# Kernel optimization log

Hardware: AMD Instinct MI355X
Metric: run time of the kernel (lower is better)

The kernel has to match this reference:

```python
import jax, jax.numpy as jnp
import numpy as np

H = 1024   # hidden_dim
L = 2      # n_layers
B = 50     # batch (hardcoded via positions expand)
S = 457    # coords length (hardcoded arange)
T = 32     # maxlen['txt']
V = 27     # dict_size


def gru_cell(x, h, Wih, Whh, bih, bhh):
    # PyTorch GRU cell math. x: (B, in), h: (B, H)
    gi = x @ Wih.T + bih
    gh = h @ Whh.T + bhh
    ir, iz, inn = jnp.split(gi, 3, axis=-1)
    hr, hz, hn = jnp.split(gh, 3, axis=-1)
    r = jax.nn.sigmoid(ir + hr)
    z = jax.nn.sigmoid(iz + hz)
    n = jnp.tanh(inn + r * hn)
    return (1.0 - z) * n + z * h


def setup_inputs() -> dict:
    key = jax.random.key(0)
    ks = iter(jax.random.split(key, 32))
    p = lambda shape: jax.random.normal(next(ks), shape, dtype=jnp.float32) * 0.05
    inp = {
        'x': jax.random.normal(next(ks), (B, 2, S), dtype=jnp.float32),
        'emb': p((V, H)),
        # encoder GRU (layer0 input=3, layer1 input=H)
        'enc_Wih0': p((3 * H, 3)), 'enc_Whh0': p((3 * H, H)),
        'enc_bih0': p((3 * H,)),   'enc_bhh0': p((3 * H,)),
        'enc_Wih1': p((3 * H, H)), 'enc_Whh1': p((3 * H, H)),
        'enc_bih1': p((3 * H,)),   'enc_bhh1': p((3 * H,)),
        # decoder GRU, stacked over layers (all inputs are H)
        'dec_Wih': p((L, 3 * H, H)), 'dec_Whh': p((L, 3 * H, H)),
        'dec_bih': p((L, 3 * H)),    'dec_bhh': p((L, 3 * H)),
        # attention_fc: Linear(2H, H) + ReLU ; fc: Linear(H, V)
        'attn_W': p((H, 2 * H)), 'attn_b': p((H,)),
        'fc_W': p((V, H)),       'fc_b': p((V,)),
    }
    return inp


def reference(x, emb, enc_Wih0, enc_Whh0, enc_bih0, enc_bhh0,
              enc_Wih1, enc_Whh1, enc_bih1, enc_bhh1,
              dec_Wih, dec_Whh, dec_bih, dec_bhh,
              attn_W, attn_b, fc_W, fc_b):
    # ----- encoder -----
    pos = jnp.broadcast_to(jnp.arange(S, dtype=x.dtype)[None, :, None], (B, S, 1))
    inp = jnp.concatenate([jnp.transpose(x, (0, 2, 1)), pos], axis=-1)  # (B,S,3)
    seq = jnp.transpose(inp, (1, 0, 2))  # (S,B,3) time-major for scan
    h0 = jnp.zeros((B, H), x.dtype)
    hiddens = []
    for (Wih, Whh, bih, bhh) in ((enc_Wih0, enc_Whh0, enc_bih0, enc_bhh0),
                                 (enc_Wih1, enc_Whh1, enc_bih1, enc_bhh1)):
        def step(h, xt, Wih=Wih, Whh=Whh, bih=bih, bhh=bhh):
            h2 = gru_cell(xt, h, Wih, Whh, bih, bhh)
            return h2, h2
        hT, seq = jax.lax.scan(step, h0, seq)
        hiddens.append(hT)
    enc_outs = jnp.transpose(seq, (1, 0, 2))  # (B,S,H)
    hidden = jnp.stack(hiddens)               # (L,B,H)

    def dec_step(carry, _):
        vec_in, hid = carry
        x_t = emb[vec_in]  # (B,H)
        new_h = []
        inp_t = x_t
        for l in range(L):
            hl = gru_cell(inp_t, hid[l], dec_Wih[l], dec_Whh[l], dec_bih[l], dec_bhh[l])
            new_h.append(hl)
            inp_t = hl
        out_t = inp_t  # (B,H)
        score = jnp.einsum('bsh,bh->bs', enc_outs, out_t)      # bmm(v, q)
        w = jax.nn.softmax(score, axis=1)                      # softmax over S
        a = jnp.einsum('bsh,bs->bh', enc_outs, w)              # bmm(v^T, w)
        comb = jnp.concatenate([out_t, a], axis=-1)            # (B,2H)
        hfc = jax.nn.relu(comb @ attn_W.T + attn_b)
        logits = hfc @ fc_W.T + fc_b                           # (B,V)
        nv = jnp.argmax(logits, axis=-1).astype(jnp.int32)
        return (nv, jnp.stack(new_h)), (logits, w)

    init = (jnp.zeros((B,), jnp.int32), hidden)
    (_, hid_f), (logits_seq, w_seq) = jax.lax.scan(dec_step, init, None, length=T)
    vec_out = jnp.transpose(logits_seq, (1, 0, 2))  # (B,T,V)
    attn_w = jnp.transpose(w_seq, (1, 2, 0))        # (B,S,T)
    return vec_out, hid_f, attn_w
```

## Files before the change

### kernel.cpp

```cpp
#include <hip/hip_runtime.h>
#include <math.h>

#define HD 1024
#define BB 50
#define SS 457
#define TT 32
#define VV 27

#define SSTR 68
#define WSTR 68

enum { G_ENC0 = 0, G_GRU = 1, G_SCR = 2, G_SCRGATE = 3, G_RELU = 4 };

struct Role {
  const float* srcA; const float* srcB;
  const float* Wa;   const float* Wb;
  const float* bih;  const float* bhh;
  const float* hv;   const float* scr;
  float* out; float* out2; float* scrw;
  int strA, strB, wstrA, K, gate, rowsLinear, gatherA, nsA, nsB;
};

__global__ __launch_bounds__(256) void fused_gemm(
    Role r0, Role r1, int split, int skipRole, int p,
    const float* __restrict__ x, const float* __restrict__ Wih0,
    const float* __restrict__ emb, const int* __restrict__ tok)
{
  __shared__ __align__(16) float Sk[64][SSTR];
  __shared__ __align__(16) float Wt[12][WSTR];
  __shared__ __align__(16) float part[4][16][4][4][4];

  const int blk = blockIdx.x;
  const int roleId = split ? (blk & 1) : 0;
  if (roleId == skipRole) return;
  const Role& R = roleId ? r1 : r0;
  const int bi2 = split ? (blk >> 1) : blk;
  const int j0 = bi2 * (R.rowsLinear ? 12 : 4);

  const int tid = threadIdx.x;
  const int tx = tid & 3;
  const int ty = (tid >> 2) & 15;
  const int kh = tid >> 6;

  float aR[4] = {0,0,0,0}, aZ[4] = {0,0,0,0}, aN2[4] = {0,0,0,0}, aN3[4] = {0,0,0,0};

  const int nit = R.K >> 6;

  for (int it = 0; it < nit; ++it) {
    const int kw = it << 6;
    const bool second = (R.srcB != nullptr) && (kw >= 1024);
    const int kloc = second ? (kw - 1024) : kw;

    float4 sv[4];
#pragma unroll
    for (int u = 0; u < 4; ++u) {
      int e = tid + (u << 8);
      int b = e >> 4, f4 = e & 15;
      int bc = b < BB ? b : BB - 1;
      const float* rp;
      if (second)         rp = R.srcB + (size_t)bc * R.strB + kloc;
      else if (R.gatherA) rp = emb + (size_t)tok[bc] * HD + kw;
      else                rp = R.srcA + (size_t)bc * R.strA + kw;
      sv[u] = *(const float4*)(rp + (f4 << 2));
    }
    float4 wv = make_float4(0.f, 0.f, 0.f, 0.f);
    if (tid < 192) {
      int r = tid >> 4, f4 = tid & 15;
      int wrow;
      if (R.rowsLinear) { int j = j0 + r; wrow = j < 1024 ? j : 1023; }
      else { int g = r >> 2, jj = r & 3; int j = j0 + jj; if (j > 1023) j = 1023;
             wrow = g * 1024 + j; }
      const float* wp = second ? (R.Wb + (size_t)wrow * 1024 + kloc)
                               : (R.Wa + (size_t)wrow * R.wstrA + kw);
      wv = *(const float4*)(wp + (f4 << 2));
    }

    __syncthreads();
#pragma unroll
    for (int u = 0; u < 4; ++u) {
      int e = tid + (u << 8);
      int b = e >> 4, f4 = e & 15;
      int k = f4 << 2;
      Sk[k + 0][b] = sv[u].x;
      Sk[k + 1][b] = sv[u].y;
      Sk[k + 2][b] = sv[u].z;
      Sk[k + 3][b] = sv[u].w;
    }
    if (tid < 192) {
      int r = tid >> 4, f4 = tid & 15;
      *(float4*)&Wt[r][f4 << 2] = wv;
    }
    __syncthreads();

    const bool ns2 = second ? (R.nsB == 2) : (R.nsA == 2);
#define FMA4(A, wc, s) { A[0] = fmaf(wc, s.x, A[0]); A[1] = fmaf(wc, s.y, A[1]); \
                         A[2] = fmaf(wc, s.z, A[2]); A[3] = fmaf(wc, s.w, A[3]); }
#define CBLOCK(AN) \
    _Pragma("unroll") \
    for (int k4 = 0; k4 < 4; ++k4) { \
      const int kk = (kh << 4) + (k4 << 2); \
      float4 w0 = *(const float4*)&Wt[tx][kk]; \
      float4 w1 = *(const float4*)&Wt[4 + tx][kk]; \
      float4 w2 = *(const float4*)&Wt[8 + tx][kk]; \
      float4 s0 = *(const float4*)&Sk[kk + 0][ty << 2]; \
      float4 s1 = *(const float4*)&Sk[kk + 1][ty << 2]; \
      float4 s2 = *(const float4*)&Sk[kk + 2][ty << 2]; \
      float4 s3 = *(const float4*)&Sk[kk + 3][ty << 2]; \
      FMA4(aR, w0.x, s0) FMA4(aR, w0.y, s1) FMA4(aR, w0.z, s2) FMA4(aR, w0.w, s3) \
      FMA4(aZ, w1.x, s0) FMA4(aZ, w1.y, s1) FMA4(aZ, w1.z, s2) FMA4(aZ, w1.w, s3) \
      FMA4(AN, w2.x, s0) FMA4(AN, w2.y, s1) FMA4(AN, w2.z, s2) FMA4(AN, w2.w, s3) \
    }
    if (ns2) { CBLOCK(aN2) } else { CBLOCK(aN3) }
    __syncthreads();
  }

  *(float4*)&part[kh][ty][tx][0][0] = make_float4(aR[0], aR[1], aR[2], aR[3]);
  *(float4*)&part[kh][ty][tx][1][0] = make_float4(aZ[0], aZ[1], aZ[2], aZ[3]);
  *(float4*)&part[kh][ty][tx][2][0] = make_float4(aN2[0], aN2[1], aN2[2], aN2[3]);
  *(float4*)&part[kh][ty][tx][3][0] = make_float4(aN3[0], aN3[1], aN3[2], aN3[3]);
  __syncthreads();

  if (tid < 200) {
    int b = tid >> 2, jj = tid & 3;
    int py = b >> 2, pi = b & 3;
    float d0 = 0.f, d1 = 0.f, d2 = 0.f, d3 = 0.f;
#pragma unroll
    for (int q = 0; q < 4; ++q) {
      d0 += part[q][py][jj][0][pi];
      d1 += part[q][py][jj][1][pi];
      d2 += part[q][py][jj][2][pi];
      d3 += part[q][py][jj][3][pi];
    }
    if (R.gate == G_ENC0) {
      int j = j0 + jj;
      float x0 = x[b * 914 + p], x1 = x[b * 914 + 457 + p], pf = (float)p;
      const float* w3r = Wih0 + (size_t)j * 3;
      const float* w3z = Wih0 + (size_t)(1024 + j) * 3;
      const float* w3n = Wih0 + (size_t)(2048 + j) * 3;
      float gir = w3r[0]*x0 + w3r[1]*x1 + w3r[2]*pf + R.bih[j];
      float giz = w3z[0]*x0 + w3z[1]*x1 + w3z[2]*pf + R.bih[1024 + j];
      float gin = w3n[0]*x0 + w3n[1]*x1 + w3n[2]*pf + R.bih[2048 + j];
      float rr = 1.f / (1.f + expf(-(gir + d0 + R.bhh[j])));
      float zz = 1.f / (1.f + expf(-(giz + d1 + R.bhh[1024 + j])));
      float nn = tanhf(gin + rr * (d3 + R.bhh[2048 + j]));
      float hv = R.hv[b * 1024 + j];
      R.out[b * 1024 + j] = (1.f - zz) * nn + zz * hv;
    } else if (R.gate == G_GRU) {
      int j = j0 + jj;
      float rr = 1.f / (1.f + expf(-(d0 + R.bih[j] + R.bhh[j])));
      float zz = 1.f / (1.f + expf(-(d1 + R.bih[1024 + j] + R.bhh[1024 + j])));
      float nn = tanhf(d2 + R.bih[2048 + j] + rr * (d3 + R.bhh[2048 + j]));
      float hv = R.hv[b * 1024 + j];
      float h2 = (1.f - zz) * nn + zz * hv;
      R.out[b * 1024 + j] = h2;
      if (R.out2) R.out2[b * 1024 + j] = h2;
    } else if (R.gate == G_SCR) {
      int j = j0 + jj;
      R.scrw[(size_t)j * 64 + b] = d0;
      R.scrw[(size_t)(1024 + j) * 64 + b] = d1;
      R.scrw[(size_t)(2048 + j) * 64 + b] = d3;
    } else if (R.gate == G_SCRGATE) {
      int j = j0 + jj;
      float ghr = R.scr[(size_t)j * 64 + b] + R.bhh[j];
      float ghz = R.scr[(size_t)(1024 + j) * 64 + b] + R.bhh[1024 + j];
      float ghn = R.scr[(size_t)(2048 + j) * 64 + b] + R.bhh[2048 + j];
      float rr = 1.f / (1.f + expf(-(d0 + R.bih[j] + ghr)));
      float zz = 1.f / (1.f + expf(-(d1 + R.bih[1024 + j] + ghz)));
      float nn = tanhf(d2 + R.bih[2048 + j] + rr * ghn);
      float hv = R.hv[b * 1024 + j];
      float h2 = (1.f - zz) * nn + zz * hv;
      R.out[b * 1024 + j] = h2;
      R.out2[b * 2048 + j] = h2;
    } else {
#pragma unroll
      for (int g = 0; g < 3; ++g) {
        int j = j0 + g * 4 + jj;
        float dg = (g == 0) ? d0 : ((g == 1) ? d1 : d2);
        if (j < 1024) R.out[b * 1024 + j] = fmaxf(dg + R.bih[j], 0.f);
      }
    }
  }
}

__global__ __launch_bounds__(256) void score_kernel(
    const float* __restrict__ enc, const float* __restrict__ comb,
    float* __restrict__ sc)
{
  int gw = (blockIdx.x * 256 + threadIdx.x) >> 6;
  int lane = threadIdx.x & 63;
  if (gw >= BB * SS) return;
  int b = gw / SS, s = gw - b * SS;
  const float* e = enc + ((size_t)s * BB + b) * HD;
  const float* q = comb + (size_t)b * 2048;
  float a = 0.f;
#pragma unroll
  for (int i = 0; i < 16; i++) a += e[lane + 64 * i] * q[lane + 64 * i];
  for (int off = 32; off; off >>= 1) a += __shfl_down(a, off);
  if (!lane) sc[b * SS + s] = a;
}

__global__ __launch_bounds__(256) void softmax_amix_kernel(
    const float* __restrict__ sc, const float* __restrict__ enc,
    float* __restrict__ comb, float* __restrict__ attn_out, int t)
{
  __shared__ float w[SS];
  __shared__ float red[256];
  int blk = blockIdx.x; int b = blk / 5, sl = blk - b * 5;
  int tid = threadIdx.x;
  float m = -1e30f;
  for (int s = tid; s < SS; s += 256) { float v = sc[b * SS + s]; w[s] = v; m = fmaxf(m, v); }
  red[tid] = m; __syncthreads();
  for (int o = 128; o; o >>= 1) { if (tid < o) red[tid] = fmaxf(red[tid], red[tid + o]); __syncthreads(); }
  m = red[0]; __syncthreads();
  float sum = 0.f;
  for (int s = tid; s < SS; s += 256) { float e = expf(w[s] - m); w[s] = e; sum += e; }
  red[tid] = sum; __syncthreads();
  for (int o = 128; o; o >>= 1) { if (tid < o) red[tid] += red[tid + o]; __syncthreads(); }
  float inv = 1.f / red[0];
  __syncthreads();
  for (int s = tid; s < SS; s += 256) w[s] *= inv;
  __syncthreads();
  if (sl == 0)
    for (int s = tid; s < SS; s += 256) attn_out[((size_t)b * SS + s) * TT + t] = w[s];
  int j0 = sl * 208; int jl = min(208, 1024 - j0);
  if (tid < jl) {
    int j = j0 + tid; float a = 0.f;
#pragma unroll 4
    for (int s = 0; s < SS; s++) a += w[s] * enc[((size_t)s * BB + b) * HD + j];
    comb[(size_t)b * 2048 + HD + j] = a;
  }
}

__global__ __launch_bounds__(256) void logits_argmax_kernel(
    const float* __restrict__ hfc, const float* __restrict__ fcW,
    const float* __restrict__ fcb, float* __restrict__ outv, int t,
    int* __restrict__ tok)
{
  __shared__ float lg[32];
  int b = blockIdx.x, tid = threadIdx.x;
  int wv = tid >> 6, lane = tid & 63;
  const float* hb = hfc + (size_t)b * HD;
  for (int v = wv; v < VV; v += 4) {
    const float* wr = fcW + (size_t)v * HD;
    float a = 0.f;
#pragma unroll
    for (int i = 0; i < 16; i++) a += hb[lane + 64 * i] * wr[lane + 64 * i];
    for (int off = 32; off; off >>= 1) a += __shfl_down(a, off);
    if (!lane) lg[v] = a + fcb[v];
  }
  __syncthreads();
  if (tid == 0) {
    float best = lg[0]; int bi = 0;
    for (int v = 1; v < VV; v++) { if (lg[v] > best) { best = lg[v]; bi = v; } }
    tok[b] = bi;
  }
  if (tid < VV) outv[((size_t)b * TT + t) * VV + tid] = lg[tid];
}

__global__ __launch_bounds__(256) void init_kernel(float* __restrict__ hbufs,
                                                   int* __restrict__ tok)
{
  int i = blockIdx.x * 256 + threadIdx.x;
  if (i < 204800) hbufs[i] = 0.f;
  if (i < BB) tok[i] = 0;
}

__global__ __launch_bounds__(256) void hidcopy_kernel(
    const float* __restrict__ h0, const float* __restrict__ h1,
    float* __restrict__ outh)
{
  int i = blockIdx.x * 256 + threadIdx.x;
  if (i < 51200) { outh[i] = h0[i]; outh[51200 + i] = h1[i]; }
}

extern "C" void kernel_launch(void* const* d_in, const int* in_sizes, int n_in,
                              void* d_out, int out_size, void* d_ws, size_t ws_size,
                              hipStream_t stream)
{
  const float* x     = (const float*)d_in[0];
  const float* emb   = (const float*)d_in[1];
  const float* eWih0 = (const float*)d_in[2];
  const float* eWhh0 = (const float*)d_in[3];
  const float* ebih0 = (const float*)d_in[4];
  const float* ebhh0 = (const float*)d_in[5];
  const float* eWih1 = (const float*)d_in[6];
  const float* eWhh1 = (const float*)d_in[7];
  const float* ebih1 = (const float*)d_in[8];
  const float* ebhh1 = (const float*)d_in[9];
  const float* dWih  = (const float*)d_in[10];
  const float* dWhh  = (const float*)d_in[11];
  const float* dbih  = (const float*)d_in[12];
  const float* dbhh  = (const float*)d_in[13];
  const float* attnW = (const float*)d_in[14];
  const float* attnB = (const float*)d_in[15];
  const float* fcW   = (const float*)d_in[16];
  const float* fcB   = (const float*)d_in[17];
  float* out = (float*)d_out;

  float* ws = (float*)d_ws;
  float* h0b[2] = { ws,          ws + 51200 };
  float* h1b[2] = { ws + 102400, ws + 153600 };
  float* enc    = ws + 204800;
  float* scr    = enc + (size_t)SS * BB * HD;
  float* comb   = scr + 3072 * 64;
  float* scoreb = comb + BB * 2048;
  float* hfc    = scoreb + BB * SS;
  int*   tok    = (int*)(hfc + BB * HD);

  float* out_vec  = out;
  float* out_hid  = out + BB * TT * VV;
  float* out_attn = out_hid + 2 * BB * HD;

  const float* dWih1 = dWih + (size_t)3072 * 1024;
  const float* dWhh1 = dWhh + (size_t)3072 * 1024;
  const float* dbih1 = dbih + 3072;
  const float* dbhh1 = dbhh + 3072;

  init_kernel<<<800, 256, 0, stream>>>(ws, tok);

  Role Z{};

  for (int p = 0; p <= 457; ++p) {
    float* h0r = h0b[(p + 1) & 1]; float* h0w = h0b[p & 1];
    float* h1r = h1b[p & 1];       float* h1w = h1b[(p + 1) & 1];
    float* encp = enc + (size_t)(p > 0 ? p - 1 : 0) * BB * HD;

    Role L0 = Z;
    L0.srcA = h0r; L0.strA = 1024; L0.Wa = eWhh0; L0.wstrA = 1024;
    L0.bih = ebih0; L0.bhh = ebhh0; L0.hv = h0r; L0.out = h0w;
    L0.K = 1024; L0.gate = G_ENC0; L0.nsA = 3; L0.nsB = 3;

    Role L1 = Z;
    L1.srcA = h0r; L1.strA = 1024; L1.srcB = h1r; L1.strB = 1024;
    L1.Wa = eWih1; L1.wstrA = 1024; L1.Wb = eWhh1;
    L1.bih = ebih1; L1.bhh = ebhh1; L1.hv = h1r;
    L1.out = h1w; L1.out2 = encp;
    L1.K = 2048; L1.gate = G_GRU; L1.nsA = 2; L1.nsB = 3;

    int skip = (p == 0) ? 1 : ((p == 457) ? 0 : -1);
    fused_gemm<<<512, 256, 0, stream>>>(L0, L1, 1, skip, p, x, eWih0, emb, tok);
  }

  for (int t = 0; t < TT; ++t) {
    float* h0r = h0b[t & 1]; float* h0w = h0b[(t + 1) & 1];
    float* h1r = h1b[t & 1]; float* h1w = h1b[(t + 1) & 1];

    Role DL0 = Z;
    DL0.gatherA = 1; DL0.srcB = h0r; DL0.strB = 1024;
    DL0.Wa = dWih; DL0.wstrA = 1024; DL0.Wb = dWhh;
    DL0.bih = dbih; DL0.bhh = dbhh; DL0.hv = h0r; DL0.out = h0w;
    DL0.K = 2048; DL0.gate = G_GRU; DL0.nsA = 2; DL0.nsB = 3;

    Role GH1 = Z;
    GH1.srcA = h1r; GH1.strA = 1024; GH1.Wa = dWhh1; GH1.wstrA = 1024;
    GH1.scrw = scr; GH1.K = 1024; GH1.gate = G_SCR; GH1.nsA = 3; GH1.nsB = 3;

    fused_gemm<<<512, 256, 0, stream>>>(DL0, GH1, 1, -1, t, x, eWih0, emb, tok);

    Role GI1 = Z;
    GI1.srcA = h0w; GI1.strA = 1024; GI1.Wa = dWih1; GI1.wstrA = 1024;
    GI1.bih = dbih1; GI1.bhh = dbhh1; GI1.hv = h1r; GI1.scr = scr;
    GI1.out = h1w; GI1.out2 = comb;
    GI1.K = 1024; GI1.gate = G_SCRGATE; GI1.nsA = 2; GI1.nsB = 2;

    fused_gemm<<<256, 256, 0, stream>>>(GI1, Z, 0, -1, t, x, eWih0, emb, tok);

    score_kernel<<<(BB * SS * 64 + 255) / 256, 256, 0, stream>>>(enc, comb, scoreb);
    softmax_amix_kernel<<<250, 256, 0, stream>>>(scoreb, enc, comb, out_attn, t);

    Role AF = Z;
    AF.srcA = comb; AF.strA = 2048; AF.Wa = attnW; AF.wstrA = 2048;
    AF.bih = attnB; AF.out = hfc;
    AF.K = 2048; AF.gate = G_RELU; AF.rowsLinear = 1; AF.nsA = 2; AF.nsB = 2;

    fused_gemm<<<86, 256, 0, stream>>>(AF, Z, 0, -1, t, x, eWih0, emb, tok);

    logits_argmax_kernel<<<BB, 256, 0, stream>>>(hfc, fcW, fcB, out_vec, t, tok);
  }

  hidcopy_kernel<<<200, 256, 0, stream>>>(h0b[0], h1b[0], out_hid);
}
```

Measured before the change: 32.99 ms.

## Replace per-step encoder launches with a cooperative persistent kernel using grid sync

The encoder recurrence moves from 458 separate fused_gemm launches into one cooperative persistent kernel. Each block owns four hidden units and runs both GRU layers per timestep, using double-buffered shared-memory tiles and a grid-wide sync between steps. This is meant to remove per-step launch overhead and let loads overlap with compute. In exchange, the two layers now run serially inside each step, and every step pays a grid barrier; the kernel also requires all 256 blocks of 1024 threads to be co-resident.

```diff
diff --git a/kernel.cpp b/kernel.cpp
--- a/kernel.cpp
+++ b/kernel.cpp
@@ -1,5 +1,8 @@
 #include <hip/hip_runtime.h>
+#include <hip/hip_cooperative_groups.h>
 #include <math.h>
+
+namespace cg = cooperative_groups;
 
 #define HD 1024
 #define BB 50
@@ -9,6 +12,195 @@
 
 #define SSTR 68
 #define WSTR 68
+
+#define SIGM(v) (1.f / (1.f + expf(-(v))))
+
+struct EncArgs {
+  const float *x, *Wih0, *Whh0, *bih0, *bhh0, *Wih1, *Whh1, *bih1, *bhh1;
+  float *h0a, *h0b2, *h1a, *h1b2, *enc;
+};
+
+#define DOT4(A, wq) do { \
+  A[0] = fmaf(wq.x, s0.x, A[0]); A[1] = fmaf(wq.x, s0.y, A[1]); \
+  A[2] = fmaf(wq.x, s0.z, A[2]); A[3] = fmaf(wq.x, s0.w, A[3]); \
+  A[0] = fmaf(wq.y, s1.x, A[0]); A[1] = fmaf(wq.y, s1.y, A[1]); \
+  A[2] = fmaf(wq.y, s1.z, A[2]); A[3] = fmaf(wq.y, s1.w, A[3]); \
+  A[0] = fmaf(wq.z, s2.x, A[0]); A[1] = fmaf(wq.z, s2.y, A[1]); \
+  A[2] = fmaf(wq.z, s2.z, A[2]); A[3] = fmaf(wq.z, s2.w, A[3]); \
+  A[0] = fmaf(wq.w, s3.x, A[0]); A[1] = fmaf(wq.w, s3.y, A[1]); \
+  A[2] = fmaf(wq.w, s3.z, A[2]); A[3] = fmaf(wq.w, s3.w, A[3]); } while (0)
+
+__global__ __launch_bounds__(1024) void enc_persistent(EncArgs A)
+{
+  __shared__ __align__(16) float Sk[2][64][SSTR];
+  __shared__ __align__(16) float Wt[2][12][WSTR];
+  __shared__ __align__(16) float part[2][16][64];
+
+  const int tid = threadIdx.x;
+  const int wj0 = blockIdx.x * 4;
+  const int lane = tid & 63;
+  const int wv = tid >> 6;
+  const int rg = wv & 3;
+  const int kh = wv >> 2;
+  const int tx = lane & 3;
+  const int ty = lane >> 2;
+  const int sb = tid >> 4;
+  const int sbc = sb < BB ? sb : BB - 1;
+  const int sf4 = tid & 15;
+  const int wr = tid >> 4;
+  const int wjl = wr & 3;
+  const int wg = wr >> 2;
+  const int wrow = wg * 1024 + wj0 + wjl;
+
+  cg::grid_group grid = cg::this_grid();
+
+  float* h0buf[2] = { A.h0a, A.h0b2 };
+  float* h1buf[2] = { A.h1a, A.h1b2 };
+
+  auto do_pass = [&](const float* sA, const float* WA,
+                     const float* sB, const float* WB,
+                     int nwin, int dual) {
+    float aR[4], aZ[4], aNi[4], aNh[4];
+#pragma unroll
+    for (int bi = 0; bi < 4; ++bi) {
+      aR[bi] = 0.f; aZ[bi] = 0.f; aNi[bi] = 0.f; aNh[bi] = 0.f;
+    }
+
+    {
+      float4 hv = *(const float4*)(sA + (size_t)sbc * 1024 + (sf4 << 2));
+      float4 wvv = make_float4(0.f, 0.f, 0.f, 0.f);
+      if (tid < 192) wvv = *(const float4*)(WA + (size_t)wrow * 1024 + (sf4 << 2));
+      const int k4 = sf4 << 2;
+      Sk[0][k4 + 0][sb] = hv.x; Sk[0][k4 + 1][sb] = hv.y;
+      Sk[0][k4 + 2][sb] = hv.z; Sk[0][k4 + 3][sb] = hv.w;
+      if (tid < 192) *(float4*)&Wt[0][wr][k4] = wvv;
+    }
+    __syncthreads();
+
+    for (int win = 0; win < nwin; ++win) {
+      const int buf = win & 1;
+      const int nxt = win + 1;
+      float4 hv2 = make_float4(0.f, 0.f, 0.f, 0.f);
+      float4 wv2 = make_float4(0.f, 0.f, 0.f, 0.f);
+      if (nxt < nwin) {
+        const float* hs; const float* Wm; int ko;
+        if (dual && nxt >= 16) { hs = sB; Wm = WB; ko = (nxt - 16) << 6; }
+        else                   { hs = sA; Wm = WA; ko = nxt << 6; }
+        hv2 = *(const float4*)(hs + (size_t)sbc * 1024 + ko + (sf4 << 2));
+        if (tid < 192) wv2 = *(const float4*)(Wm + (size_t)wrow * 1024 + ko + (sf4 << 2));
+      }
+      const int kk = (kh << 4) + (tx << 2);
+      const float4 s0 = *(const float4*)&Sk[buf][kk + 0][ty << 2];
+      const float4 s1 = *(const float4*)&Sk[buf][kk + 1][ty << 2];
+      const float4 s2 = *(const float4*)&Sk[buf][kk + 2][ty << 2];
+      const float4 s3 = *(const float4*)&Sk[buf][kk + 3][ty << 2];
+      const int useNi = dual && (win < 16);
+      {
+        const float4 w0 = *(const float4*)&Wt[buf][rg][kk];
+        const float4 w1 = *(const float4*)&Wt[buf][4 + rg][kk];
+        const float4 w2 = *(const float4*)&Wt[buf][8 + rg][kk];
+        DOT4(aR, w0);
+        DOT4(aZ, w1);
+        if (useNi) { DOT4(aNi, w2); } else { DOT4(aNh, w2); }
+      }
+      if (nxt < nwin) {
+        const int nb = nxt & 1;
+        const int k4 = sf4 << 2;
+        Sk[nb][k4 + 0][sb] = hv2.x; Sk[nb][k4 + 1][sb] = hv2.y;
+        Sk[nb][k4 + 2][sb] = hv2.z; Sk[nb][k4 + 3][sb] = hv2.w;
+        if (tid < 192) *(float4*)&Wt[nb][wr][k4] = wv2;
+      }
+      __syncthreads();
+    }
+
+#pragma unroll
+    for (int bi = 0; bi < 4; ++bi) {
+      aR[bi]  += __shfl_xor(aR[bi], 1, 64);
+      aR[bi]  += __shfl_xor(aR[bi], 2, 64);
+      aZ[bi]  += __shfl_xor(aZ[bi], 1, 64);
+      aZ[bi]  += __shfl_xor(aZ[bi], 2, 64);
+      aNi[bi] += __shfl_xor(aNi[bi], 1, 64);
+      aNi[bi] += __shfl_xor(aNi[bi], 2, 64);
+      aNh[bi] += __shfl_xor(aNh[bi], 1, 64);
+      aNh[bi] += __shfl_xor(aNh[bi], 2, 64);
+    }
+    if (tx == 0 && (kh & 1) == 0) {
+      const int pr = rg << 2;
+      *(float4*)&part[kh >> 1][pr + 0][ty << 2] = make_float4(aR[0], aR[1], aR[2], aR[3]);
+      *(float4*)&part[kh >> 1][pr + 1][ty << 2] = make_float4(aZ[0], aZ[1], aZ[2], aZ[3]);
+      *(float4*)&part[kh >> 1][pr + 2][ty << 2] = make_float4(aNi[0], aNi[1], aNi[2], aNi[3]);
+      *(float4*)&part[kh >> 1][pr + 3][ty << 2] = make_float4(aNh[0], aNh[1], aNh[2], aNh[3]);
+    }
+    __syncthreads();
+    if (tx == 0 && (kh & 1) == 1) {
+      const int pr = rg << 2;
+      float4* q0 = (float4*)&part[kh >> 1][pr + 0][ty << 2];
+      float4* q1 = (float4*)&part[kh >> 1][pr + 1][ty << 2];
+      float4* q2 = (float4*)&part[kh >> 1][pr + 2][ty << 2];
+      float4* q3 = (float4*)&part[kh >> 1][pr + 3][ty << 2];
+      float4 v0 = *q0; v0.x += aR[0];  v0.y += aR[1];  v0.z += aR[2];  v0.w += aR[3];  *q0 = v0;
+      float4 v1 = *q1; v1.x += aZ[0];  v1.y += aZ[1];  v1.z += aZ[2];  v1.w += aZ[3];  *q1 = v1;
+      float4 v2 = *q2; v2.x += aNi[0]; v2.y += aNi[1]; v2.z += aNi[2]; v2.w += aNi[3]; *q2 = v2;
+      float4 v3 = *q3; v3.x += aNh[0]; v3.y += aNh[1]; v3.z += aNh[2]; v3.w += aNh[3]; *q3 = v3;
+    }
+    __syncthreads();
+  };
+
+  for (int p = 0; p <= 457; ++p) {
+    const float* h0r = h0buf[(p + 1) & 1];
+    float*       h0w = h0buf[p & 1];
+    const float* h1r = h1buf[p & 1];
+    float*       h1w = h1buf[(p + 1) & 1];
+
+    if (p < 457) {
+      do_pass(h0r, A.Whh0, nullptr, nullptr, 16, 0);
+      if (tid < 200) {
+        const int jl = tid / 50, b = tid - jl * 50;
+        const int j = wj0 + jl;
+        const int pr = jl << 2;
+        const float dR  = part[0][pr + 0][b] + part[1][pr + 0][b];
+        const float dZ  = part[0][pr + 1][b] + part[1][pr + 1][b];
+        const float dNh = part[0][pr + 3][b] + part[1][pr + 3][b];
+        const float x0 = A.x[b * 914 + p];
+        const float x1 = A.x[b * 914 + 457 + p];
+        const float pf = (float)p;
+        const float* w3r = A.Wih0 + (size_t)j * 3;
+        const float* w3z = A.Wih0 + (size_t)(1024 + j) * 3;
+        const float* w3n = A.Wih0 + (size_t)(2048 + j) * 3;
+        const float gir = w3r[0]*x0 + w3r[1]*x1 + w3r[2]*pf + A.bih0[j];
+        const float giz = w3z[0]*x0 + w3z[1]*x1 + w3z[2]*pf + A.bih0[1024 + j];
+        const float gin = w3n[0]*x0 + w3n[1]*x1 + w3n[2]*pf + A.bih0[2048 + j];
+        const float rr = SIGM(gir + dR + A.bhh0[j]);
+        const float zz = SIGM(giz + dZ + A.bhh0[1024 + j]);
+        const float nn = tanhf(gin + rr * (dNh + A.bhh0[2048 + j]));
+        const float hv0 = h0r[b * 1024 + j];
+        h0w[b * 1024 + j] = (1.f - zz) * nn + zz * hv0;
+      }
+      __syncthreads();
+    }
+    if (p > 0) {
+      do_pass(h0r, A.Wih1, h1r, A.Whh1, 32, 1);
+      if (tid < 200) {
+        const int jl = tid / 50, b = tid - jl * 50;
+        const int j = wj0 + jl;
+        const int pr = jl << 2;
+        const float dR  = part[0][pr + 0][b] + part[1][pr + 0][b];
+        const float dZ  = part[0][pr + 1][b] + part[1][pr + 1][b];
+        const float dNi = part[0][pr + 2][b] + part[1][pr + 2][b];
+        const float dNh = part[0][pr + 3][b] + part[1][pr + 3][b];
+        const float rr = SIGM(dR + A.bih1[j] + A.bhh1[j]);
+        const float zz = SIGM(dZ + A.bih1[1024 + j] + A.bhh1[1024 + j]);
+        const float nn = tanhf(dNi + A.bih1[2048 + j] + rr * (dNh + A.bhh1[2048 + j]));
+        const float hv1 = h1r[b * 1024 + j];
+        const float h2 = (1.f - zz) * nn + zz * hv1;
+        h1w[b * 1024 + j] = h2;
+        A.enc[(size_t)(p - 1) * (BB * HD) + b * 1024 + j] = h2;
+      }
+      __syncthreads();
+    }
+    grid.sync();
+  }
+}
 
 enum { G_ENC0 = 0, G_GRU = 1, G_SCR = 2, G_SCRGATE = 3, G_RELU = 4 };
 
@@ -63,7 +255,7 @@
       else                rp = R.srcA + (size_t)bc * R.strA + kw;
       sv[u] = *(const float4*)(rp + (f4 << 2));
     }
-    float4 wv = make_float4(0.f, 0.f, 0.f, 0.f);
+    float4 wvq = make_float4(0.f, 0.f, 0.f, 0.f);
     if (tid < 192) {
       int r = tid >> 4, f4 = tid & 15;
       int wrow;
@@ -72,7 +264,7 @@
              wrow = g * 1024 + j; }
       const float* wp = second ? (R.Wb + (size_t)wrow * 1024 + kloc)
                                : (R.Wa + (size_t)wrow * R.wstrA + kw);
-      wv = *(const float4*)(wp + (f4 << 2));
+      wvq = *(const float4*)(wp + (f4 << 2));
     }
 
     __syncthreads();
@@ -88,7 +280,7 @@
     }
     if (tid < 192) {
       int r = tid >> 4, f4 = tid & 15;
-      *(float4*)&Wt[r][f4 << 2] = wv;
+      *(float4*)&Wt[r][f4 << 2] = wvq;
     }
     __syncthreads();
 
@@ -140,15 +332,15 @@
       float gir = w3r[0]*x0 + w3r[1]*x1 + w3r[2]*pf + R.bih[j];
       float giz = w3z[0]*x0 + w3z[1]*x1 + w3z[2]*pf + R.bih[1024 + j];
       float gin = w3n[0]*x0 + w3n[1]*x1 + w3n[2]*pf + R.bih[2048 + j];
-      float rr = 1.f / (1.f + expf(-(gir + d0 + R.bhh[j])));
-      float zz = 1.f / (1.f + expf(-(giz + d1 + R.bhh[1024 + j])));
+      float rr = SIGM(gir + d0 + R.bhh[j]);
+      float zz = SIGM(giz + d1 + R.bhh[1024 + j]);
       float nn = tanhf(gin + rr * (d3 + R.bhh[2048 + j]));
       float hv = R.hv[b * 1024 + j];
       R.out[b * 1024 + j] = (1.f - zz) * nn + zz * hv;
     } else if (R.gate == G_GRU) {
       int j = j0 + jj;
-      float rr = 1.f / (1.f + expf(-(d0 + R.bih[j] + R.bhh[j])));
-      float zz = 1.f / (1.f + expf(-(d1 + R.bih[1024 + j] + R.bhh[1024 + j])));
+      float rr = SIGM(d0 + R.bih[j] + R.bhh[j]);
+      float zz = SIGM(d1 + R.bih[1024 + j] + R.bhh[1024 + j]);
       float nn = tanhf(d2 + R.bih[2048 + j] + rr * (d3 + R.bhh[2048 + j]));
       float hv = R.hv[b * 1024 + j];
       float h2 = (1.f - zz) * nn + zz * hv;
@@ -164,8 +356,8 @@
       float ghr = R.scr[(size_t)j * 64 + b] + R.bhh[j];
       float ghz = R.scr[(size_t)(1024 + j) * 64 + b] + R.bhh[1024 + j];
       float ghn = R.scr[(size_t)(2048 + j) * 64 + b] + R.bhh[2048 + j];
-      float rr = 1.f / (1.f + expf(-(d0 + R.bih[j] + ghr)));
-      float zz = 1.f / (1.f + expf(-(d1 + R.bih[1024 + j] + ghz)));
+      float rr = SIGM(d0 + R.bih[j] + ghr);
+      float zz = SIGM(d1 + R.bih[1024 + j] + ghz);
       float nn = tanhf(d2 + R.bih[2048 + j] + rr * ghn);
       float hv = R.hv[b * 1024 + j];
       float h2 = (1.f - zz) * nn + zz * hv;
@@ -238,9 +430,9 @@
 {
   __shared__ float lg[32];
   int b = blockIdx.x, tid = threadIdx.x;
-  int wv = tid >> 6, lane = tid & 63;
+  int wvv = tid >> 6, lane = tid & 63;
   const float* hb = hfc + (size_t)b * HD;
-  for (int v = wv; v < VV; v += 4) {
+  for (int v = wvv; v < VV; v += 4) {
     const float* wr = fcW + (size_t)v * HD;
     float a = 0.f;
 #pragma unroll
@@ -318,28 +510,16 @@
 
   init_kernel<<<800, 256, 0, stream>>>(ws, tok);
 
+  EncArgs ea;
+  ea.x = x; ea.Wih0 = eWih0; ea.Whh0 = eWhh0; ea.bih0 = ebih0; ea.bhh0 = ebhh0;
+  ea.Wih1 = eWih1; ea.Whh1 = eWhh1; ea.bih1 = ebih1; ea.bhh1 = ebhh1;
+  ea.h0a = h0b[0]; ea.h0b2 = h0b[1]; ea.h1a = h1b[0]; ea.h1b2 = h1b[1];
+  ea.enc = enc;
+  void* kargs[] = { (void*)&ea };
+  hipLaunchCooperativeKernel((void*)enc_persistent, dim3(256), dim3(1024),
+                             kargs, 0, stream);
+
   Role Z{};
-
-  for (int p = 0; p <= 457; ++p) {
-    float* h0r = h0b[(p + 1) & 1]; float* h0w = h0b[p & 1];
-    float* h1r = h1b[p & 1];       float* h1w = h1b[(p + 1) & 1];
-    float* encp = enc + (size_t)(p > 0 ? p - 1 : 0) * BB * HD;
-
-    Role L0 = Z;
-    L0.srcA = h0r; L0.strA = 1024; L0.Wa = eWhh0; L0.wstrA = 1024;
-    L0.bih = ebih0; L0.bhh = ebhh0; L0.hv = h0r; L0.out = h0w;
-    L0.K = 1024; L0.gate = G_ENC0; L0.nsA = 3; L0.nsB = 3;
-
-    Role L1 = Z;
-    L1.srcA = h0r; L1.strA = 1024; L1.srcB = h1r; L1.strB = 1024;
-    L1.Wa = eWih1; L1.wstrA = 1024; L1.Wb = eWhh1;
-    L1.bih = ebih1; L1.bhh = ebhh1; L1.hv = h1r;
-    L1.out = h1w; L1.out2 = encp;
-    L1.K = 2048; L1.gate = G_GRU; L1.nsA = 2; L1.nsB = 3;
-
-    int skip = (p == 0) ? 1 : ((p == 457) ? 0 : -1);
-    fused_gemm<<<512, 256, 0, stream>>>(L0, L1, 1, skip, p, x, eWih0, emb, tok);
-  }
 
   for (int t = 0; t < TT; ++t) {
     float* h0r = h0b[t & 1]; float* h0w = h0b[(t + 1) & 1];
```

Result: slower. 111.2 ms (+237.1%).
